# Kernel optimization log

Measured on AMD Instinct MI355X. Metric: run time of the kernel, lower is better.

The kernel has to match this reference:

```python
import jax, jax.numpy as jnp
import numpy as np

H = 4  # num_heads

def setup_inputs() -> dict:
    key = jax.random.key(0)
    ks = jax.random.split(key, 9)
    B, S, D = 8, 2048, 256
    x = jax.random.normal(ks[0], (B, S, D), dtype=jnp.float32)
    scale = 1.0 / np.sqrt(D)
    Wq = jax.random.normal(ks[1], (D, D), dtype=jnp.float32) * scale
    bq = jnp.zeros((D,), dtype=jnp.float32)
    Wk = jax.random.normal(ks[2], (D, D), dtype=jnp.float32) * scale
    bk = jnp.zeros((D,), dtype=jnp.float32)
    Wv = jax.random.normal(ks[3], (D, D), dtype=jnp.float32) * scale
    bv = jnp.zeros((D,), dtype=jnp.float32)
    Wo = jax.random.normal(ks[4], (D, D), dtype=jnp.float32) * scale
    bo = jnp.zeros((D,), dtype=jnp.float32)
    return {"x": x, "Wq": Wq, "bq": bq, "Wk": Wk, "bk": bk,
            "Wv": Wv, "bv": bv, "Wo": Wo, "bo": bo}

def reference(x, Wq, bq, Wk, bk, Wv, bv, Wo, bo):
    B, S, D = x.shape
    hd = D // H
    inv_scale = 1.0 / jnp.sqrt(jnp.asarray(hd, x.dtype))
    # projections: torch Linear is x @ W.T + b; weights here stored as (D, D) used as x @ W + b
    def split_heads(t):
        return t.reshape(B, S, H, hd).transpose(0, 2, 1, 3)  # [B,H,S,hd]
    Q = split_heads(x @ Wq + bq)
    K = split_heads(x @ Wk + bk)
    V = split_heads(x @ Wv + bv)
    scores = jnp.einsum('bhqd,bhkd->bhqk', Q, K) * inv_scale  # [B,H,S,S]
    attn = jax.nn.softmax(scores, axis=-1)
    # dropout is identity in eval mode
    ctx = jnp.einsum('bhqk,bhkd->bhqd', attn, V)
    ctx = ctx.transpose(0, 2, 1, 3).reshape(B, S, D)
    return ctx @ Wo + bo
```

## Files before the change

### kernel.cpp

```cpp
#include <hip/hip_runtime.h>


typedef unsigned short u16;
typedef __bf16 bf16x8 __attribute__((ext_vector_type(8)));
typedef float  f32x4  __attribute__((ext_vector_type(4)));
typedef unsigned int u32x4 __attribute__((ext_vector_type(4)));
typedef unsigned int u32x2 __attribute__((ext_vector_type(2)));

#define LOG2E   1.4426950408889634f
#define ATTN_SC (0.125f * LOG2E)
#define PSTR    2097152
#define WPSTR   32768
#define WZSTR   65536

__device__ __forceinline__ u16 f2b(float f) {
  unsigned u = __builtin_bit_cast(unsigned, f);
  u += 0x7FFFu + ((u >> 16) & 1u);
  return (u16)(u >> 16);
}
__device__ __forceinline__ float b2f(u16 b) {
  return __builtin_bit_cast(float, (unsigned)b << 16);
}
__device__ __forceinline__ unsigned pack_trunc(float a, float b) {
  return (__builtin_bit_cast(unsigned, a) >> 16) | (__builtin_bit_cast(unsigned, b) & 0xFFFF0000u);
}
__device__ __forceinline__ unsigned pack_rne(float a, float b) {
  return (unsigned)f2b(a) | ((unsigned)f2b(b) << 16);
}
__device__ __forceinline__ f32x4 mfma16(bf16x8 a, bf16x8 b, f32x4 c) {
  return __builtin_amdgcn_mfma_f32_16x16x32_bf16(a, b, c, 0, 0, 0);
}
__device__ __forceinline__ void cp16(const u16* g, u16* l) {
  __builtin_amdgcn_global_load_lds((const __attribute__((address_space(1))) void*)g,
                                   (__attribute__((address_space(3))) void*)l, 16, 0, 0);
}

template <typename T>
__global__ __launch_bounds__(256) void prep(const T* __restrict__ x,
                                            const T* __restrict__ W0, const T* __restrict__ W1,
                                            const T* __restrict__ W2, const T* __restrict__ W3,
                                            const T* __restrict__ b0, const T* __restrict__ b1,
                                            const T* __restrict__ b2, const T* __restrict__ b3,
                                            u16* __restrict__ xp, u16* __restrict__ WTp,
                                            float* __restrict__ biasf) {
  int bid = blockIdx.x;
  if (bid < 4096) {
    int i0 = (bid * 256 + threadIdx.x) * 4;
    int row = i0 >> 8, col = i0 & 255;
    int p = col >> 7, pc = col & 127;
    u16* o = xp + (size_t)p * PSTR + (size_t)row * 128 + pc;
#pragma unroll
    for (int j = 0; j < 4; ++j) {
      if constexpr (sizeof(T) == 4) o[j] = f2b((float)x[i0 + j]);
      else                          o[j] = (u16)x[i0 + j];
    }
  } else {
    bid -= 4096;
    const int z = bid >> 8;
    const T* W = z == 0 ? W0 : z == 1 ? W1 : z == 2 ? W2 : W3;
    const T* b = z == 0 ? b0 : z == 1 ? b1 : z == 2 ? b2 : b3;
    int idx = (bid & 255) * 256 + threadIdx.x;
    int k = idx >> 8, n = idx & 255;
    u16 wb;
    if constexpr (sizeof(T) == 4) wb = f2b((float)W[k * 256 + n]);
    else                          wb = (u16)W[k * 256 + n];
    WTp[z * WZSTR + (k >> 7) * WPSTR + n * 128 + (k & 127)] = wb;
    if (idx < 256) {
      float bv;
      if constexpr (sizeof(T) == 4) bv = (float)b[idx];
      else                          bv = b2f((u16)b[idx]);
      biasf[z * 256 + idx] = bv;
    }
  }
}

__device__ __forceinline__ void gemm_body(const u16* Ab, const u16* Bb,
                                          u16* Al, u16* Bl, f32x4 acc[2][4], int tid) {
  const int w = tid >> 6, lane = tid & 63;
  const int l16 = lane & 15, quad = lane >> 4;
#pragma unroll
  for (int p = 0; p < 2; ++p) {
    __syncthreads();
    const u16* Ap = Ab + (size_t)p * PSTR;
    const u16* Bp = Bb + p * WPSTR;
#pragma unroll
    for (int i = 0; i < 8; ++i) {
      int slot = i * 256 + w * 64 + lane;
      int row = slot >> 4, pc = slot & 15, c = pc ^ (row & 15);
      cp16(Ap + (size_t)row * 128 + c * 8, Al + (i * 256 + w * 64) * 8);
    }
#pragma unroll
    for (int i = 0; i < 4; ++i) {
      int slot = i * 256 + w * 64 + lane;
      int row = slot >> 4, pc = slot & 15, c = pc ^ (row & 15);
      cp16(Bp + (size_t)row * 128 + c * 8, Bl + (i * 256 + w * 64) * 8);
    }
    __syncthreads();
#pragma unroll
    for (int kc = 0; kc < 4; ++kc) {
      bf16x8 a0 = *(const bf16x8*)&Al[(w * 32 + l16) * 128 + (((kc * 4 + quad) ^ l16)) * 8];
      bf16x8 a1 = *(const bf16x8*)&Al[(w * 32 + 16 + l16) * 128 + (((kc * 4 + quad) ^ l16)) * 8];
#pragma unroll
      for (int nb = 0; nb < 4; ++nb) {
        bf16x8 b = *(const bf16x8*)&Bl[(nb * 16 + l16) * 128 + (((kc * 4 + quad) ^ l16)) * 8];
        acc[0][nb] = mfma16(a0, b, acc[0][nb]);
        acc[1][nb] = mfma16(a1, b, acc[1][nb]);
      }
    }
  }
}

__global__ __launch_bounds__(256) void qkv_gemm(const u16* __restrict__ xp, const u16* __restrict__ WTp,
                                                const float* __restrict__ biasf,
                                                u16* __restrict__ Qw, u16* __restrict__ Kw,
                                                u16* __restrict__ VTg) {
  __shared__ __align__(16) u16 Al[128 * 128];
  __shared__ __align__(16) u16 Bl[64 * 128];
  const int tid = threadIdx.x, w = tid >> 6, lane = tid & 63;
  const int l16 = lane & 15, quad = lane >> 4;
  const int z = blockIdx.z, n0 = blockIdx.y * 64, m0 = blockIdx.x * 128;
  f32x4 acc[2][4];
#pragma unroll
  for (int mm = 0; mm < 2; ++mm)
#pragma unroll
    for (int nb = 0; nb < 4; ++nb) acc[mm][nb] = (f32x4){0.f, 0.f, 0.f, 0.f};

  gemm_body(xp + (size_t)m0 * 128, WTp + z * WZSTR + n0 * 128, Al, Bl, acc, tid);

  const float* bp = biasf + z * 256;
  const int bb = m0 >> 11, s0 = m0 & 2047, h = blockIdx.y;
  if (z < 2) {
    u16* dst = (z == 0) ? Qw : Kw;
    const float sc = (z == 0) ? ATTN_SC : 1.0f;
#pragma unroll
    for (int mm = 0; mm < 2; ++mm)
#pragma unroll
      for (int nb = 0; nb < 4; ++nb) {
        int d = nb * 16 + l16;
        float bv = bp[n0 + d];
#pragma unroll
        for (int r = 0; r < 4; ++r) {
          int s = s0 + w * 32 + mm * 16 + quad * 4 + r;
          dst[(((size_t)(bb * 4 + h) * 2048) + s) * 64 + d] = f2b((acc[mm][nb][r] + bv) * sc);
        }
      }
  } else {
    __syncthreads();
#pragma unroll
    for (int mm = 0; mm < 2; ++mm)
#pragma unroll
      for (int nb = 0; nb < 4; ++nb) {
        int d = nb * 16 + l16;
        float bv = bp[n0 + d];
        f32x4 v = acc[mm][nb];
        u32x2 dd = { pack_rne(v[0] + bv, v[1] + bv), pack_rne(v[2] + bv, v[3] + bv) };
        int cch = w * 4 + mm * 2 + (quad >> 1);
        *(u32x2*)&Bl[d * 128 + ((cch ^ (d & 15))) * 8 + (quad & 1) * 4] = dd;
      }
    __syncthreads();
#pragma unroll
    for (int i = 0; i < 4; ++i) {
      int slot = i * 256 + tid;
      int d = slot >> 4, pc = slot & 15;
      u32x4 vv = *(const u32x4*)&Bl[d * 128 + ((pc ^ (d & 15))) * 8];
      *(u32x4*)(VTg + (((size_t)(bb * 4 + h) * 64) + d) * 2048 + s0 + pc * 8) = vv;
    }
  }
}

template <bool OUT_BF16>
__global__ __launch_bounds__(256) void out_gemm(const u16* __restrict__ ctxp, const u16* __restrict__ WTp,
                                                const float* __restrict__ bo, void* __restrict__ outv) {
  __shared__ __align__(16) u16 Al[128 * 128];
  __shared__ __align__(16) u16 Bl[64 * 128];
  const int tid = threadIdx.x, w = tid >> 6, lane = tid & 63;
  const int l16 = lane & 15, quad = lane >> 4;
  const int n0 = blockIdx.y * 64, m0 = blockIdx.x * 128;
  f32x4 acc[2][4];
#pragma unroll
  for (int mm = 0; mm < 2; ++mm)
#pragma unroll
    for (int nb = 0; nb < 4; ++nb) acc[mm][nb] = (f32x4){0.f, 0.f, 0.f, 0.f};

  gemm_body(ctxp + (size_t)m0 * 128, WTp + 3 * WZSTR + n0 * 128, Al, Bl, acc, tid);

#pragma unroll
  for (int mm = 0; mm < 2; ++mm)
#pragma unroll
    for (int nb = 0; nb < 4; ++nb) {
      int n = n0 + nb * 16 + l16;
      float bv = bo[n];
#pragma unroll
      for (int r = 0; r < 4; ++r) {
        size_t m = m0 + w * 32 + mm * 16 + quad * 4 + r;
        float v = acc[mm][nb][r] + bv;
        if constexpr (OUT_BF16) ((u16*)outv)[m * 256 + n] = f2b(v);
        else                    ((float*)outv)[m * 256 + n] = v;
      }
    }
}

__global__ __launch_bounds__(256, 2) void attn(const u16* __restrict__ Q, const u16* __restrict__ K,
                                               const u16* __restrict__ VT, u16* __restrict__ ctxp) {
  __shared__ __align__(16) u16 Kt[2][64 * 64];
  __shared__ __align__(16) u16 VTt[2][64 * 64];
  __shared__ __align__(16) u16 Pt[4][16 * 64];
  const int tid = threadIdx.x;
  const int w = tid >> 6, lane = tid & 63;
  const int l16 = lane & 15, quad = lane >> 4;
  const int bh = blockIdx.y, q0 = blockIdx.x * 128;
  const u16* Qp = Q + (size_t)bh * 2048 * 64;
  const u16* Kp = K + (size_t)bh * 2048 * 64;
  const u16* Vp = VT + (size_t)bh * 64 * 2048;
  u16* Ptw = Pt[w];

  bf16x8 qf[2][2];
#pragma unroll
  for (int h = 0; h < 2; ++h) {
    int qrow = q0 + w * 32 + h * 16 + l16;
    qf[h][0] = *(const bf16x8*)(Qp + (size_t)qrow * 64 + quad * 8);
    qf[h][1] = *(const bf16x8*)(Qp + (size_t)qrow * 64 + 32 + quad * 8);
  }

  f32x4 acc[2][4];
#pragma unroll
  for (int h = 0; h < 2; ++h)
#pragma unroll
    for (int nb = 0; nb < 4; ++nb) acc[h][nb] = (f32x4){0.f, 0.f, 0.f, 0.f};
  float dn0 = 0.f, dn1 = 0.f;

  const int sl0 = w * 64 + lane, sl1 = 256 + w * 64 + lane;
  const int r0 = sl0 >> 3, c0 = (sl0 & 7) ^ (r0 & 7);
  const int r1 = sl1 >> 3, c1 = (sl1 & 7) ^ (r1 & 7);
  const int pr0 = (r0 & 0x20) | ((r0 & 0x0C) << 1) | ((r0 & 0x10) >> 2) | (r0 & 3);
  const int pr1 = (r1 & 0x20) | ((r1 & 0x0C) << 1) | ((r1 & 0x10) >> 2) | (r1 & 3);

#define STAGE(kt_, buf_)                                                               \
  do {                                                                                 \
    cp16(Kp + (size_t)((kt_) * 64 + pr0) * 64 + c0 * 8, &Kt[buf_][(w * 64) * 8]);      \
    cp16(Kp + (size_t)((kt_) * 64 + pr1) * 64 + c1 * 8, &Kt[buf_][(256 + w * 64) * 8]);\
    cp16(Vp + (size_t)r0 * 2048 + (kt_) * 64 + c0 * 8, &VTt[buf_][(w * 64) * 8]);      \
    cp16(Vp + (size_t)r1 * 2048 + (kt_) * 64 + c1 * 8, &VTt[buf_][(256 + w * 64) * 8]);\
  } while (0)

  STAGE(0, 0);

  for (int kt = 0; kt < 32; ++kt) {
    const int buf = kt & 1;
    __builtin_amdgcn_s_waitcnt(0x0F70 );
    __asm__ __volatile__("" ::: "memory");
    __builtin_amdgcn_s_barrier();
    __asm__ __volatile__("" ::: "memory");
    if (kt < 31) STAGE(kt + 1, buf ^ 1);

    const u16* KtB = Kt[buf];
    const u16* VtB = VTt[buf];

    bf16x8 kfr[2][4];
#pragma unroll
    for (int kc = 0; kc < 2; ++kc)
#pragma unroll
      for (int nbK = 0; nbK < 4; ++nbK)
        kfr[kc][nbK] = *(const bf16x8*)&KtB[(nbK * 16 + l16) * 64 + (((kc * 4 + quad) ^ (l16 & 7))) * 8];
    bf16x8 vbr[2][4];
#pragma unroll
    for (int m = 0; m < 2; ++m)
#pragma unroll
      for (int nbD = 0; nbD < 4; ++nbD)
        vbr[m][nbD] = *(const bf16x8*)&VtB[(nbD * 16 + l16) * 64 + (((m * 4 + quad) ^ (l16 & 7))) * 8];

#pragma unroll
    for (int h = 0; h < 2; ++h) {
      f32x4 st[4];
#pragma unroll
      for (int nb = 0; nb < 4; ++nb) st[nb] = (f32x4){0.f, 0.f, 0.f, 0.f};
#pragma unroll
      for (int kc = 0; kc < 2; ++kc)
#pragma unroll
        for (int nbK = 0; nbK < 4; ++nbK)
          st[nbK] = mfma16(kfr[kc][nbK], qf[h][kc], st[nbK]);

      unsigned pw[8];
      float d = 0.f;
#pragma unroll
      for (int nbK = 0; nbK < 4; ++nbK) {
        float p0 = __builtin_amdgcn_exp2f(st[nbK][0]);
        float p1 = __builtin_amdgcn_exp2f(st[nbK][1]);
        float p2 = __builtin_amdgcn_exp2f(st[nbK][2]);
        float p3 = __builtin_amdgcn_exp2f(st[nbK][3]);
        d += (p0 + p1) + (p2 + p3);
        pw[nbK * 2]     = pack_trunc(p0, p1);
        pw[nbK * 2 + 1] = pack_trunc(p2, p3);
      }
      if (h == 0) dn0 += d; else dn1 += d;
      bf16x8 pb0 = __builtin_bit_cast(bf16x8, (u32x4){pw[0], pw[1], pw[2], pw[3]});
      bf16x8 pb1 = __builtin_bit_cast(bf16x8, (u32x4){pw[4], pw[5], pw[6], pw[7]});

#pragma unroll
      for (int nbD = 0; nbD < 4; ++nbD) acc[h][nbD] = mfma16(vbr[0][nbD], pb0, acc[h][nbD]);
#pragma unroll
      for (int nbD = 0; nbD < 4; ++nbD) acc[h][nbD] = mfma16(vbr[1][nbD], pb1, acc[h][nbD]);
    }
  }
#undef STAGE

  float linv0, linv1;
  { float d = dn0; d += __shfl_xor(d, 16); d += __shfl_xor(d, 32); linv0 = 1.0f / d; }
  { float d = dn1; d += __shfl_xor(d, 16); d += __shfl_xor(d, 32); linv1 = 1.0f / d; }

  const int bb = bh >> 2, hh = bh & 3;
  const int p = hh >> 1, pcol = (hh & 1) * 64;
#pragma unroll
  for (int h = 0; h < 2; ++h) {
    const float linv = h ? linv1 : linv0;
#pragma unroll
    for (int nbD = 0; nbD < 4; ++nbD) {
      f32x4 v = acc[h][nbD];
      u32x2 dd = { pack_rne(v[0] * linv, v[1] * linv), pack_rne(v[2] * linv, v[3] * linv) };
      int cch = nbD * 2 + (quad >> 1);
      *(u32x2*)&Ptw[l16 * 64 + ((cch ^ (l16 & 7))) * 8 + (quad & 1) * 4] = dd;
    }
    __asm__ __volatile__("" ::: "memory");
#pragma unroll
    for (int cc = 0; cc < 2; ++cc) {
      int slot = cc * 64 + lane;
      int row = slot >> 3, pc = slot & 7;
      u32x4 vv = *(const u32x4*)&Ptw[row * 64 + ((pc ^ (row & 7))) * 8];
      size_t m = (size_t)bb * 2048 + q0 + w * 32 + h * 16 + row;
      *(u32x4*)&ctxp[(size_t)p * PSTR + m * 128 + pcol + pc * 8] = vv;
    }
    __asm__ __volatile__("" ::: "memory");
  }
}

extern "C" void kernel_launch(void* const* d_in, const int* in_sizes, int n_in,
                              void* d_out, int out_size, void* d_ws, size_t ws_size,
                              hipStream_t stream) {
  bool f32in = true;
  {
    void* basep = nullptr; size_t sz = 0;
    hipError_t e = hipMemGetAddressRange((hipDeviceptr_t*)&basep, &sz, (hipDeviceptr_t)d_in[0]);
    if (e == hipSuccess && sz > 0) f32in = sz >= (size_t)in_sizes[0] * 4;
    else f32in = false;
  }

  char* ws = (char*)d_ws;
  u16*   xp    = (u16*)(ws + 0);
  u16*   ctxp  = xp;
  u16*   WTp   = (u16*)(ws + 8388608);
  float* biasf = (float*)(ws + 8912896);
  u16*   Qw    = (u16*)(ws + 8916992);
  u16*   Kw    = (u16*)(ws + 17305600);
  u16*   VTg   = (u16*)(ws + 25694208);

  dim3 blk(256);
  if (f32in) {
    prep<float><<<5120, blk, 0, stream>>>(
        (const float*)d_in[0],
        (const float*)d_in[1], (const float*)d_in[3], (const float*)d_in[5], (const float*)d_in[7],
        (const float*)d_in[2], (const float*)d_in[4], (const float*)d_in[6], (const float*)d_in[8],
        xp, WTp, biasf);
  } else {
    prep<u16><<<5120, blk, 0, stream>>>(
        (const u16*)d_in[0],
        (const u16*)d_in[1], (const u16*)d_in[3], (const u16*)d_in[5], (const u16*)d_in[7],
        (const u16*)d_in[2], (const u16*)d_in[4], (const u16*)d_in[6], (const u16*)d_in[8],
        xp, WTp, biasf);
  }
  qkv_gemm<<<dim3(128, 4, 3), blk, 0, stream>>>(xp, WTp, biasf, Qw, Kw, VTg);
  attn<<<dim3(16, 32), blk, 0, stream>>>(Qw, Kw, VTg, ctxp);
  if (f32in) out_gemm<false><<<dim3(128, 4), blk, 0, stream>>>(ctxp, WTp, biasf + 3 * 256, d_out);
  else       out_gemm<true ><<<dim3(128, 4), blk, 0, stream>>>(ctxp, WTp, biasf + 3 * 256, d_out);
}
```

Measured before the change: 150.6 us.

## Halve attention block to 2 waves per 64 queries and add MFMA priority hints

The attention kernel now runs 128-thread blocks covering 64 query rows, which doubles the grid to 32x32 blocks. Each wave now issues four async copies per K/V tile instead of two. s_setprio is raised around the MFMA sections so matrix work is favoured over other waves' exp/pack work. A barrier is added before the epilogue reuses the smaller Pt buffer. More blocks improve occupancy and load balance across CUs, but each K/V tile is loaded by more blocks, which increases global/L2 traffic.

```diff
diff --git a/kernel.cpp b/kernel.cpp
--- a/kernel.cpp
+++ b/kernel.cpp
@@ -200,15 +200,15 @@
     }
 }
 
-__global__ __launch_bounds__(256, 2) void attn(const u16* __restrict__ Q, const u16* __restrict__ K,
+__global__ __launch_bounds__(128, 2) void attn(const u16* __restrict__ Q, const u16* __restrict__ K,
                                                const u16* __restrict__ VT, u16* __restrict__ ctxp) {
   __shared__ __align__(16) u16 Kt[2][64 * 64];
   __shared__ __align__(16) u16 VTt[2][64 * 64];
-  __shared__ __align__(16) u16 Pt[4][16 * 64];
+  __shared__ __align__(16) u16 Pt[2][16 * 64];
   const int tid = threadIdx.x;
   const int w = tid >> 6, lane = tid & 63;
   const int l16 = lane & 15, quad = lane >> 4;
-  const int bh = blockIdx.y, q0 = blockIdx.x * 128;
+  const int bh = blockIdx.y, q0 = blockIdx.x * 64;
   const u16* Qp = Q + (size_t)bh * 2048 * 64;
   const u16* Kp = K + (size_t)bh * 2048 * 64;
   const u16* Vp = VT + (size_t)bh * 64 * 2048;
@@ -229,18 +229,25 @@
     for (int nb = 0; nb < 4; ++nb) acc[h][nb] = (f32x4){0.f, 0.f, 0.f, 0.f};
   float dn0 = 0.f, dn1 = 0.f;
 
-  const int sl0 = w * 64 + lane, sl1 = 256 + w * 64 + lane;
-  const int r0 = sl0 >> 3, c0 = (sl0 & 7) ^ (r0 & 7);
-  const int r1 = sl1 >> 3, c1 = (sl1 & 7) ^ (r1 & 7);
-  const int pr0 = (r0 & 0x20) | ((r0 & 0x0C) << 1) | ((r0 & 0x10) >> 2) | (r0 & 3);
-  const int pr1 = (r1 & 0x20) | ((r1 & 0x0C) << 1) | ((r1 & 0x10) >> 2) | (r1 & 3);
-
-#define STAGE(kt_, buf_)                                                               \
-  do {                                                                                 \
-    cp16(Kp + (size_t)((kt_) * 64 + pr0) * 64 + c0 * 8, &Kt[buf_][(w * 64) * 8]);      \
-    cp16(Kp + (size_t)((kt_) * 64 + pr1) * 64 + c1 * 8, &Kt[buf_][(256 + w * 64) * 8]);\
-    cp16(Vp + (size_t)r0 * 2048 + (kt_) * 64 + c0 * 8, &VTt[buf_][(w * 64) * 8]);      \
-    cp16(Vp + (size_t)r1 * 2048 + (kt_) * 64 + c1 * 8, &VTt[buf_][(256 + w * 64) * 8]);\
+  int rr[4], cc[4], pr[4];
+#pragma unroll
+  for (int i = 0; i < 4; ++i) {
+    int sl = i * 128 + w * 64 + lane;
+    rr[i] = sl >> 3;
+    cc[i] = (sl & 7) ^ (rr[i] & 7);
+    pr[i] = (rr[i] & 0x20) | ((rr[i] & 0x0C) << 1) | ((rr[i] & 0x10) >> 2) | (rr[i] & 3);
+  }
+
+#define STAGE(kt_, buf_)                                                                   \
+  do {                                                                                     \
+    _Pragma("unroll")                                                                      \
+    for (int i = 0; i < 4; ++i)                                                            \
+      cp16(Kp + (size_t)((kt_) * 64 + pr[i]) * 64 + cc[i] * 8,                             \
+           &Kt[buf_][(i * 128 + w * 64) * 8]);                                             \
+    _Pragma("unroll")                                                                      \
+    for (int i = 0; i < 4; ++i)                                                            \
+      cp16(Vp + (size_t)rr[i] * 2048 + (kt_) * 64 + cc[i] * 8,                             \
+           &VTt[buf_][(i * 128 + w * 64) * 8]);                                            \
   } while (0)
 
   STAGE(0, 0);
@@ -274,11 +281,13 @@
       f32x4 st[4];
 #pragma unroll
       for (int nb = 0; nb < 4; ++nb) st[nb] = (f32x4){0.f, 0.f, 0.f, 0.f};
+      __builtin_amdgcn_s_setprio(1);
 #pragma unroll
       for (int kc = 0; kc < 2; ++kc)
 #pragma unroll
         for (int nbK = 0; nbK < 4; ++nbK)
           st[nbK] = mfma16(kfr[kc][nbK], qf[h][kc], st[nbK]);
+      __builtin_amdgcn_s_setprio(0);
 
       unsigned pw[8];
       float d = 0.f;
@@ -296,10 +305,12 @@
       bf16x8 pb0 = __builtin_bit_cast(bf16x8, (u32x4){pw[0], pw[1], pw[2], pw[3]});
       bf16x8 pb1 = __builtin_bit_cast(bf16x8, (u32x4){pw[4], pw[5], pw[6], pw[7]});
 
+      __builtin_amdgcn_s_setprio(1);
 #pragma unroll
       for (int nbD = 0; nbD < 4; ++nbD) acc[h][nbD] = mfma16(vbr[0][nbD], pb0, acc[h][nbD]);
 #pragma unroll
       for (int nbD = 0; nbD < 4; ++nbD) acc[h][nbD] = mfma16(vbr[1][nbD], pb1, acc[h][nbD]);
+      __builtin_amdgcn_s_setprio(0);
     }
   }
 #undef STAGE
@@ -308,6 +319,9 @@
   { float d = dn0; d += __shfl_xor(d, 16); d += __shfl_xor(d, 32); linv0 = 1.0f / d; }
   { float d = dn1; d += __shfl_xor(d, 16); d += __shfl_xor(d, 32); linv1 = 1.0f / d; }
 
+  __asm__ __volatile__("" ::: "memory");
+  __builtin_amdgcn_s_barrier();
+  __asm__ __volatile__("" ::: "memory");
   const int bb = bh >> 2, hh = bh & 3;
   const int p = hh >> 1, pcol = (hh & 1) * 64;
 #pragma unroll
@@ -322,8 +336,8 @@
     }
     __asm__ __volatile__("" ::: "memory");
 #pragma unroll
-    for (int cc = 0; cc < 2; ++cc) {
-      int slot = cc * 64 + lane;
+    for (int cc2 = 0; cc2 < 2; ++cc2) {
+      int slot = cc2 * 64 + lane;
       int row = slot >> 3, pc = slot & 7;
       u32x4 vv = *(const u32x4*)&Ptw[row * 64 + ((pc ^ (row & 7))) * 8];
       size_t m = (size_t)bb * 2048 + q0 + w * 32 + h * 16 + row;
@@ -368,7 +382,7 @@
         xp, WTp, biasf);
   }
   qkv_gemm<<<dim3(128, 4, 3), blk, 0, stream>>>(xp, WTp, biasf, Qw, Kw, VTg);
-  attn<<<dim3(16, 32), blk, 0, stream>>>(Qw, Kw, VTg, ctxp);
+  attn<<<dim3(32, 32), dim3(128), 0, stream>>>(Qw, Kw, VTg, ctxp);
   if (f32in) out_gemm<false><<<dim3(128, 4), blk, 0, stream>>>(ctxp, WTp, biasf + 3 * 256, d_out);
   else       out_gemm<true ><<<dim3(128, 4), blk, 0, stream>>>(ctxp, WTp, biasf + 3 * 256, d_out);
 }
```

Result: slower. 156.0 us (+3.6%).

## Fuse Q/K/V projections per block and widen output GEMM N-tile

Applied to the files above, without the earlier changes.

The QKV GEMM now computes all three projections in one block, loading the x tile once and reusing it against three weight tiles, which removes the z grid dimension and cuts redundant A-tile loads. The output GEMM doubles its N tile to 128 so each A tile is reused across more columns, halving its grid. Both raise LDS use and per-thread accumulator registers, and the grids shrink (512 and 256 blocks), which may lower occupancy and parallelism on a many-CU GPU.

```diff
diff --git a/kernel.cpp b/kernel.cpp
--- a/kernel.cpp
+++ b/kernel.cpp
@@ -74,15 +74,27 @@
   }
 }
 
-__device__ __forceinline__ void gemm_body(const u16* Ab, const u16* Bb,
-                                          u16* Al, u16* Bl, f32x4 acc[2][4], int tid) {
-  const int w = tid >> 6, lane = tid & 63;
+__global__ __launch_bounds__(256, 2) void qkv_gemm(const u16* __restrict__ xp, const u16* __restrict__ WTp,
+                                                   const float* __restrict__ biasf,
+                                                   u16* __restrict__ Qw, u16* __restrict__ Kw,
+                                                   u16* __restrict__ VTg) {
+  __shared__ __align__(16) u16 Al[128 * 128];
+  __shared__ __align__(16) u16 Bl[3][64 * 128];
+  const int tid = threadIdx.x, w = tid >> 6, lane = tid & 63;
   const int l16 = lane & 15, quad = lane >> 4;
+  const int n0 = blockIdx.y * 64, m0 = blockIdx.x * 128;
+  f32x4 acc[3][2][4];
+#pragma unroll
+  for (int z = 0; z < 3; ++z)
+#pragma unroll
+    for (int mm = 0; mm < 2; ++mm)
+#pragma unroll
+      for (int nb = 0; nb < 4; ++nb) acc[z][mm][nb] = (f32x4){0.f, 0.f, 0.f, 0.f};
+
 #pragma unroll
   for (int p = 0; p < 2; ++p) {
     __syncthreads();
-    const u16* Ap = Ab + (size_t)p * PSTR;
-    const u16* Bp = Bb + p * WPSTR;
+    const u16* Ap = xp + (size_t)m0 * 128 + (size_t)p * PSTR;
 #pragma unroll
     for (int i = 0; i < 8; ++i) {
       int slot = i * 256 + w * 64 + lane;
@@ -90,7 +102,102 @@
       cp16(Ap + (size_t)row * 128 + c * 8, Al + (i * 256 + w * 64) * 8);
     }
 #pragma unroll
+    for (int z = 0; z < 3; ++z) {
+      const u16* Bp = WTp + z * WZSTR + n0 * 128 + p * WPSTR;
+#pragma unroll
+      for (int i = 0; i < 4; ++i) {
+        int slot = i * 256 + w * 64 + lane;
+        int row = slot >> 4, pc = slot & 15, c = pc ^ (row & 15);
+        cp16(Bp + (size_t)row * 128 + c * 8, Bl[z] + (i * 256 + w * 64) * 8);
+      }
+    }
+    __syncthreads();
+#pragma unroll
+    for (int kc = 0; kc < 4; ++kc) {
+      bf16x8 a0 = *(const bf16x8*)&Al[(w * 32 + l16) * 128 + (((kc * 4 + quad) ^ l16)) * 8];
+      bf16x8 a1 = *(const bf16x8*)&Al[(w * 32 + 16 + l16) * 128 + (((kc * 4 + quad) ^ l16)) * 8];
+#pragma unroll
+      for (int z = 0; z < 3; ++z)
+#pragma unroll
+        for (int nb = 0; nb < 4; ++nb) {
+          bf16x8 b = *(const bf16x8*)&Bl[z][(nb * 16 + l16) * 128 + (((kc * 4 + quad) ^ l16)) * 8];
+          acc[z][0][nb] = mfma16(a0, b, acc[z][0][nb]);
+          acc[z][1][nb] = mfma16(a1, b, acc[z][1][nb]);
+        }
+    }
+  }
+
+  const int bb = m0 >> 11, s0 = m0 & 2047, h = blockIdx.y;
+#pragma unroll
+  for (int z = 0; z < 2; ++z) {
+    u16* dst = (z == 0) ? Qw : Kw;
+    const float sc = (z == 0) ? ATTN_SC : 1.0f;
+    const float* bp = biasf + z * 256;
+#pragma unroll
+    for (int mm = 0; mm < 2; ++mm)
+#pragma unroll
+      for (int nb = 0; nb < 4; ++nb) {
+        int d = nb * 16 + l16;
+        float bv = bp[n0 + d];
+#pragma unroll
+        for (int r = 0; r < 4; ++r) {
+          int s = s0 + w * 32 + mm * 16 + quad * 4 + r;
+          dst[(((size_t)(bb * 4 + h) * 2048) + s) * 64 + d] = f2b((acc[z][mm][nb][r] + bv) * sc);
+        }
+      }
+  }
+  __syncthreads();
+  {
+    const float* bp = biasf + 2 * 256;
+#pragma unroll
+    for (int mm = 0; mm < 2; ++mm)
+#pragma unroll
+      for (int nb = 0; nb < 4; ++nb) {
+        int d = nb * 16 + l16;
+        float bv = bp[n0 + d];
+        f32x4 v = acc[2][mm][nb];
+        u32x2 dd = { pack_rne(v[0] + bv, v[1] + bv), pack_rne(v[2] + bv, v[3] + bv) };
+        int cch = w * 4 + mm * 2 + (quad >> 1);
+        *(u32x2*)&Bl[0][d * 128 + ((cch ^ (d & 15))) * 8 + (quad & 1) * 4] = dd;
+      }
+    __syncthreads();
+#pragma unroll
     for (int i = 0; i < 4; ++i) {
+      int slot = i * 256 + tid;
+      int d = slot >> 4, pc = slot & 15;
+      u32x4 vv = *(const u32x4*)&Bl[0][d * 128 + ((pc ^ (d & 15))) * 8];
+      *(u32x4*)(VTg + (((size_t)(bb * 4 + h) * 64) + d) * 2048 + s0 + pc * 8) = vv;
+    }
+  }
+}
+
+template <bool OUT_BF16>
+__global__ __launch_bounds__(256, 2) void out_gemm(const u16* __restrict__ ctxp, const u16* __restrict__ WTp,
+                                                   const float* __restrict__ bo, void* __restrict__ outv) {
+  __shared__ __align__(16) u16 Al[128 * 128];
+  __shared__ __align__(16) u16 Bl[128 * 128];
+  const int tid = threadIdx.x, w = tid >> 6, lane = tid & 63;
+  const int l16 = lane & 15, quad = lane >> 4;
+  const int n0 = blockIdx.y * 128, m0 = blockIdx.x * 128;
+  f32x4 acc[2][8];
+#pragma unroll
+  for (int mm = 0; mm < 2; ++mm)
+#pragma unroll
+    for (int nb = 0; nb < 8; ++nb) acc[mm][nb] = (f32x4){0.f, 0.f, 0.f, 0.f};
+
+#pragma unroll
+  for (int p = 0; p < 2; ++p) {
+    __syncthreads();
+    const u16* Ap = ctxp + (size_t)m0 * 128 + (size_t)p * PSTR;
+    const u16* Bp = WTp + 3 * WZSTR + n0 * 128 + p * WPSTR;
+#pragma unroll
+    for (int i = 0; i < 8; ++i) {
+      int slot = i * 256 + w * 64 + lane;
+      int row = slot >> 4, pc = slot & 15, c = pc ^ (row & 15);
+      cp16(Ap + (size_t)row * 128 + c * 8, Al + (i * 256 + w * 64) * 8);
+    }
+#pragma unroll
+    for (int i = 0; i < 8; ++i) {
       int slot = i * 256 + w * 64 + lane;
       int row = slot >> 4, pc = slot & 15, c = pc ^ (row & 15);
       cp16(Bp + (size_t)row * 128 + c * 8, Bl + (i * 256 + w * 64) * 8);
@@ -101,93 +208,18 @@
       bf16x8 a0 = *(const bf16x8*)&Al[(w * 32 + l16) * 128 + (((kc * 4 + quad) ^ l16)) * 8];
       bf16x8 a1 = *(const bf16x8*)&Al[(w * 32 + 16 + l16) * 128 + (((kc * 4 + quad) ^ l16)) * 8];
 #pragma unroll
-      for (int nb = 0; nb < 4; ++nb) {
+      for (int nb = 0; nb < 8; ++nb) {
         bf16x8 b = *(const bf16x8*)&Bl[(nb * 16 + l16) * 128 + (((kc * 4 + quad) ^ l16)) * 8];
         acc[0][nb] = mfma16(a0, b, acc[0][nb]);
         acc[1][nb] = mfma16(a1, b, acc[1][nb]);
       }
     }
   }
-}
-
-__global__ __launch_bounds__(256) void qkv_gemm(const u16* __restrict__ xp, const u16* __restrict__ WTp,
-                                                const float* __restrict__ biasf,
-                                                u16* __restrict__ Qw, u16* __restrict__ Kw,
-                                                u16* __restrict__ VTg) {
-  __shared__ __align__(16) u16 Al[128 * 128];
-  __shared__ __align__(16) u16 Bl[64 * 128];
-  const int tid = threadIdx.x, w = tid >> 6, lane = tid & 63;
-  const int l16 = lane & 15, quad = lane >> 4;
-  const int z = blockIdx.z, n0 = blockIdx.y * 64, m0 = blockIdx.x * 128;
-  f32x4 acc[2][4];
+
 #pragma unroll
   for (int mm = 0; mm < 2; ++mm)
 #pragma unroll
-    for (int nb = 0; nb < 4; ++nb) acc[mm][nb] = (f32x4){0.f, 0.f, 0.f, 0.f};
-
-  gemm_body(xp + (size_t)m0 * 128, WTp + z * WZSTR + n0 * 128, Al, Bl, acc, tid);
-
-  const float* bp = biasf + z * 256;
-  const int bb = m0 >> 11, s0 = m0 & 2047, h = blockIdx.y;
-  if (z < 2) {
-    u16* dst = (z == 0) ? Qw : Kw;
-    const float sc = (z == 0) ? ATTN_SC : 1.0f;
-#pragma unroll
-    for (int mm = 0; mm < 2; ++mm)
-#pragma unroll
-      for (int nb = 0; nb < 4; ++nb) {
-        int d = nb * 16 + l16;
-        float bv = bp[n0 + d];
-#pragma unroll
-        for (int r = 0; r < 4; ++r) {
-          int s = s0 + w * 32 + mm * 16 + quad * 4 + r;
-          dst[(((size_t)(bb * 4 + h) * 2048) + s) * 64 + d] = f2b((acc[mm][nb][r] + bv) * sc);
-        }
-      }
-  } else {
-    __syncthreads();
-#pragma unroll
-    for (int mm = 0; mm < 2; ++mm)
-#pragma unroll
-      for (int nb = 0; nb < 4; ++nb) {
-        int d = nb * 16 + l16;
-        float bv = bp[n0 + d];
-        f32x4 v = acc[mm][nb];
-        u32x2 dd = { pack_rne(v[0] + bv, v[1] + bv), pack_rne(v[2] + bv, v[3] + bv) };
-        int cch = w * 4 + mm * 2 + (quad >> 1);
-        *(u32x2*)&Bl[d * 128 + ((cch ^ (d & 15))) * 8 + (quad & 1) * 4] = dd;
-      }
-    __syncthreads();
-#pragma unroll
-    for (int i = 0; i < 4; ++i) {
-      int slot = i * 256 + tid;
-      int d = slot >> 4, pc = slot & 15;
-      u32x4 vv = *(const u32x4*)&Bl[d * 128 + ((pc ^ (d & 15))) * 8];
-      *(u32x4*)(VTg + (((size_t)(bb * 4 + h) * 64) + d) * 2048 + s0 + pc * 8) = vv;
-    }
-  }
-}
-
-template <bool OUT_BF16>
-__global__ __launch_bounds__(256) void out_gemm(const u16* __restrict__ ctxp, const u16* __restrict__ WTp,
-                                                const float* __restrict__ bo, void* __restrict__ outv) {
-  __shared__ __align__(16) u16 Al[128 * 128];
-  __shared__ __align__(16) u16 Bl[64 * 128];
-  const int tid = threadIdx.x, w = tid >> 6, lane = tid & 63;
-  const int l16 = lane & 15, quad = lane >> 4;
-  const int n0 = blockIdx.y * 64, m0 = blockIdx.x * 128;
-  f32x4 acc[2][4];
-#pragma unroll
-  for (int mm = 0; mm < 2; ++mm)
-#pragma unroll
-    for (int nb = 0; nb < 4; ++nb) acc[mm][nb] = (f32x4){0.f, 0.f, 0.f, 0.f};
-
-  gemm_body(ctxp + (size_t)m0 * 128, WTp + 3 * WZSTR + n0 * 128, Al, Bl, acc, tid);
-
-#pragma unroll
-  for (int mm = 0; mm < 2; ++mm)
-#pragma unroll
-    for (int nb = 0; nb < 4; ++nb) {
+    for (int nb = 0; nb < 8; ++nb) {
       int n = n0 + nb * 16 + l16;
       float bv = bo[n];
 #pragma unroll
@@ -322,8 +354,8 @@
     }
     __asm__ __volatile__("" ::: "memory");
 #pragma unroll
-    for (int cc = 0; cc < 2; ++cc) {
-      int slot = cc * 64 + lane;
+    for (int cc2 = 0; cc2 < 2; ++cc2) {
+      int slot = cc2 * 64 + lane;
       int row = slot >> 3, pc = slot & 7;
       u32x4 vv = *(const u32x4*)&Ptw[row * 64 + ((pc ^ (row & 7))) * 8];
       size_t m = (size_t)bb * 2048 + q0 + w * 32 + h * 16 + row;
@@ -367,8 +399,8 @@
         (const u16*)d_in[2], (const u16*)d_in[4], (const u16*)d_in[6], (const u16*)d_in[8],
         xp, WTp, biasf);
   }
-  qkv_gemm<<<dim3(128, 4, 3), blk, 0, stream>>>(xp, WTp, biasf, Qw, Kw, VTg);
+  qkv_gemm<<<dim3(128, 4), blk, 0, stream>>>(xp, WTp, biasf, Qw, Kw, VTg);
   attn<<<dim3(16, 32), blk, 0, stream>>>(Qw, Kw, VTg, ctxp);
-  if (f32in) out_gemm<false><<<dim3(128, 4), blk, 0, stream>>>(ctxp, WTp, biasf + 3 * 256, d_out);
-  else       out_gemm<true ><<<dim3(128, 4), blk, 0, stream>>>(ctxp, WTp, biasf + 3 * 256, d_out);
-}
+  if (f32in) out_gemm<false><<<dim3(128, 2), blk, 0, stream>>>(ctxp, WTp, biasf + 3 * 256, d_out);
+  else       out_gemm<true ><<<dim3(128, 2), blk, 0, stream>>>(ctxp, WTp, biasf + 3 * 256, d_out);
+}
```

Result: faster. 146.2 us (-2.9%).
